# Kernel optimization log

Hardware: AMD Instinct MI355X
Metric: run time of the kernel (lower is better)

Reference implementation:

```python
import jax, jax.numpy as jnp
import numpy as np

NEG_SLOPE = 0.2
TAU_MRF = 1.0
N_NODES = 100000
PROJ_DIM = 128
GAT_DIM = 64
N_EDGES = 1000000


def setup_inputs() -> dict:
    key = jax.random.key(0)
    ks = jax.random.split(key, 8)
    z_beh = jax.random.normal(ks[0], (N_NODES, PROJ_DIM), dtype=jnp.float32)
    z_pref = jax.random.normal(ks[1], (N_NODES, PROJ_DIM), dtype=jnp.float32)
    edge_index = jax.random.randint(ks[2], (2, N_EDGES), 0, N_NODES, dtype=jnp.int64)
    # xavier_uniform for [GAT_DIM, PROJ_DIM] linear weights
    lim_w = float(np.sqrt(6.0 / (PROJ_DIM + GAT_DIM)))
    W_b = jax.random.uniform(ks[3], (GAT_DIM, PROJ_DIM), minval=-lim_w, maxval=lim_w, dtype=jnp.float32)
    W_p = jax.random.uniform(ks[4], (GAT_DIM, PROJ_DIM), minval=-lim_w, maxval=lim_w, dtype=jnp.float32)
    # xavier_uniform on view(1, 2D): fan_in=1? torch treats [1, 2D] -> fan_in=2D, fan_out=1
    lim_a = float(np.sqrt(6.0 / (1 + 2 * GAT_DIM)))
    a_b = jax.random.uniform(ks[5], (2 * GAT_DIM,), minval=-lim_a, maxval=lim_a, dtype=jnp.float32)
    a_p = jax.random.uniform(ks[6], (2 * GAT_DIM,), minval=-lim_a, maxval=lim_a, dtype=jnp.float32)
    gamma_b = jnp.zeros((), dtype=jnp.float32)
    gamma_p = jnp.zeros((), dtype=jnp.float32)
    return {"z_beh": z_beh, "z_pref": z_pref, "W_b": W_b, "W_p": W_p,
            "a_b": a_b, "a_p": a_p, "gamma_b": gamma_b, "gamma_p": gamma_p,
            "edge_index_undirected": edge_index}


def _sym_score(h, a, src, dst, neg_slope):
    # e_ij = leaky_relu((cat[h_src, h_dst]) . a). Split a to avoid materializing
    # the [E, 2D] concat: dot each node once, then gather scalars per edge.
    D = h.shape[-1]
    si = h @ a[:D]   # [N] contribution of left slot
    sj = h @ a[D:]   # [N] contribution of right slot
    e_ij = jax.nn.leaky_relu(si[src] + sj[dst], negative_slope=neg_slope)
    e_ji = jax.nn.leaky_relu(si[dst] + sj[src], negative_slope=neg_slope)
    return 0.5 * (e_ij + e_ji)


def reference(z_beh, z_pref, W_b, W_p, a_b, a_p, gamma_b, gamma_p, edge_index_undirected):
    src = edge_index_undirected[0]
    dst = edge_index_undirected[1]
    h_b = z_beh @ W_b.T   # [N, D]
    h_p = z_pref @ W_p.T  # [N, D]
    s_b = _sym_score(h_b, a_b, src, dst, NEG_SLOPE)  # [E]
    s_p = _sym_score(h_p, a_p, src, dst, NEG_SLOPE)  # [E]
    w = jax.nn.softmax(jnp.stack([gamma_b, gamma_p]))
    s = w[0] * s_b + w[1] * s_p
    alpha_ij = jax.nn.sigmoid(s / TAU_MRF)
    return alpha_ij
```

## Files before the change

kernel.cpp:

```cpp
#include <hip/hip_runtime.h>
#include <hip/hip_bf16.h>

#define NEG_SLOPE 0.2f

typedef float f32x4 __attribute__((ext_vector_type(4)));

__device__ __forceinline__ unsigned f2bf(float f) {
    unsigned u = __float_as_uint(f);
    return (u + 0x7FFFu + ((u >> 16) & 1u)) >> 16;
}
__device__ __forceinline__ float bf2f(unsigned h) {
    return __uint_as_float(h << 16);
}

__global__ void compute_v_kernel(const float* __restrict__ W_b,
                                 const float* __restrict__ W_p,
                                 const float* __restrict__ a_b,
                                 const float* __restrict__ a_p,
                                 float* __restrict__ v) {
    const int t  = threadIdx.x;
    const int p  = t & 127;
    const int ch = t >> 7;
    const float* W = ch ? W_p : W_b;
    const float* a = ch ? a_p : a_b;
    float acc1 = 0.f, acc2 = 0.f;
    #pragma unroll
    for (int d = 0; d < 64; ++d) {
        const float w = W[d * 128 + p];
        acc1 += w * a[d];
        acc2 += w * a[64 + d];
    }
    v[(2 * ch + 0) * 128 + p] = acc1;
    v[(2 * ch + 1) * 128 + p] = acc2;
}

__device__ __forceinline__ float fold_reduce(float sib, float sjb,
                                             float sip, float sjp,
                                             bool hiB, bool hiJ) {
    float g1 = hiB ? sib : sip;
    float r1 = __shfl_xor(g1, 16);
    float acc_i = (hiB ? sip : sib) + r1;
    float g2 = hiB ? sjb : sjp;
    float r2 = __shfl_xor(g2, 16);
    float acc_j = (hiB ? sjp : sjb) + r2;
    float g3 = hiJ ? acc_i : acc_j;
    float r3 = __shfl_xor(g3, 8);
    float acc = (hiJ ? acc_j : acc_i) + r3;
    acc += __shfl_xor(acc, 4);
    acc += __shfl_xor(acc, 2);
    acc += __shfl_xor(acc, 1);
    return acc;
}

__device__ __forceinline__ float dot4(const f32x4 z, const f32x4 v) {
    return z.x * v.x + z.y * v.y + z.z * v.z + z.w * v.w;
}

__device__ __forceinline__ void pack_store(float acc, int c, bool valid,
                                           uint2* __restrict__ tab8, int node) {
    const float a1 = __shfl_down(acc, 8);
    const float a2 = __shfl_down(acc, 16);
    const float a3 = __shfl_down(acc, 24);
    if (c == 0 && valid) {
        uint2 p;
        p.x = f2bf(acc) | (f2bf(a1) << 16);
        p.y = f2bf(a2) | (f2bf(a3) << 16);
        tab8[node] = p;
    }
}

__global__ void __launch_bounds__(256, 8) node_scores_kernel(
        const f32x4* __restrict__ zb4,
        const f32x4* __restrict__ zp4,
        const float* __restrict__ v,
        uint2*       __restrict__ tab8,
        int n_nodes) {
    const int tid  = threadIdx.x;
    const int lane = tid & 63;
    const int h    = lane >> 5;
    const int c    = lane & 31;
    const int wave   = (blockIdx.x * blockDim.x + tid) >> 6;
    const int nwaves = (gridDim.x * blockDim.x) >> 6;
    const int npairs = (n_nodes + 1) >> 1;

    const f32x4 v1b = *reinterpret_cast<const f32x4*>(v + 0 * 128 + 4 * c);
    const f32x4 v2b = *reinterpret_cast<const f32x4*>(v + 1 * 128 + 4 * c);
    const f32x4 v1p = *reinterpret_cast<const f32x4*>(v + 2 * 128 + 4 * c);
    const f32x4 v2p = *reinterpret_cast<const f32x4*>(v + 3 * 128 + 4 * c);

    const bool hiB = (c & 16) != 0;
    const bool hiJ = (c & 8)  != 0;

    for (int pr0 = wave; pr0 < npairs; pr0 += 4 * nwaves) {
        f32x4 zb[4], zp[4];
        #pragma unroll
        for (int j = 0; j < 4; ++j) {
            const int pr = pr0 + j * nwaves;
            if (pr < npairs) {
                const size_t base = (size_t)(2 * pr + h) * 32 + c;
                zb[j] = zb4[base];
                zp[j] = zp4[base];
            }
        }
        #pragma unroll
        for (int j = 0; j < 4; ++j) {
            const int pr = pr0 + j * nwaves;
            if (pr < npairs) {
                const int node = 2 * pr + h;
                const float acc = fold_reduce(
                    dot4(zb[j], v1b), dot4(zb[j], v2b),
                    dot4(zp[j], v1p), dot4(zp[j], v2p), hiB, hiJ);
                pack_store(acc, c, node < n_nodes, tab8, node);
            }
        }
    }
}

__device__ __forceinline__ float lrelu(float x) {
    return x >= 0.f ? x : NEG_SLOPE * x;
}

__device__ __forceinline__ float edge_score8(const uint2 ts, const uint2 td,
                                             float w0, float w1) {
    const float s_ib = bf2f(ts.x & 0xFFFFu), s_jb = bf2f(ts.x >> 16);
    const float s_ip = bf2f(ts.y & 0xFFFFu), s_jp = bf2f(ts.y >> 16);
    const float d_ib = bf2f(td.x & 0xFFFFu), d_jb = bf2f(td.x >> 16);
    const float d_ip = bf2f(td.y & 0xFFFFu), d_jp = bf2f(td.y >> 16);
    const float sb = 0.5f * (lrelu(s_ib + d_jb) + lrelu(d_ib + s_jb));
    const float sp = 0.5f * (lrelu(s_ip + d_jp) + lrelu(d_ip + s_jp));
    const float sc = w0 * sb + w1 * sp;
    return 1.f / (1.f + __expf(-sc));
}

__global__ void __launch_bounds__(256) edge_scores_kernel(
        const int*   __restrict__ src,
        const int*   __restrict__ dst,
        const uint2* __restrict__ tab8,
        const float* __restrict__ gamma_b,
        const float* __restrict__ gamma_p,
        float*       __restrict__ out,
        int n_edges) {
    const float gb = *gamma_b;
    const float gp = *gamma_p;
    const float w0 = 1.f / (1.f + __expf(gp - gb));
    const float w1 = 1.f - w0;

    const int n_half = n_edges >> 1;
    const int stride = gridDim.x * blockDim.x;
    const int gid    = blockIdx.x * blockDim.x + threadIdx.x;

    const int2* src2 = (const int2*)src;
    const int2* dst2 = (const int2*)dst;
    float2*     out2 = (float2*)out;

    for (int i = gid; i < n_half; i += stride) {
        const int2 s = src2[i];
        const int2 d = dst2[i];
        const uint2 ts0 = tab8[s.x];
        const uint2 td0 = tab8[d.x];
        const uint2 ts1 = tab8[s.y];
        const uint2 td1 = tab8[d.y];
        float2 r;
        r.x = edge_score8(ts0, td0, w0, w1);
        r.y = edge_score8(ts1, td1, w0, w1);
        out2[i] = r;
    }
    const int tail_base = n_half << 1;
    for (int e = tail_base + gid; e < n_edges; e += stride) {
        out[e] = edge_score8(tab8[src[e]], tab8[dst[e]], w0, w1);
    }
}

extern "C" void kernel_launch(void* const* d_in, const int* in_sizes, int n_in,
                              void* d_out, int out_size, void* d_ws, size_t ws_size,
                              hipStream_t stream) {
    const float* z_beh  = (const float*)d_in[0];
    const float* z_pref = (const float*)d_in[1];
    const float* W_b    = (const float*)d_in[2];
    const float* W_p    = (const float*)d_in[3];
    const float* a_b    = (const float*)d_in[4];
    const float* a_p    = (const float*)d_in[5];
    const float* g_b    = (const float*)d_in[6];
    const float* g_p    = (const float*)d_in[7];
    const int*   ei     = (const int*)d_in[8];

    const int n_nodes = in_sizes[0] / 128;
    const int n_edges = in_sizes[8] / 2;

    float* v    = (float*)d_ws;
    uint2* tab8 = (uint2*)((char*)d_ws + 2048);

    compute_v_kernel<<<1, 256, 0, stream>>>(W_b, W_p, a_b, a_p, v);

    node_scores_kernel<<<2048, 256, 0, stream>>>(
        (const f32x4*)z_beh, (const f32x4*)z_pref, v, tab8, n_nodes);

    const int n_half = n_edges >> 1;
    int eblocks = (n_half + 255) / 256;
    if (eblocks > 4096) eblocks = 4096;
    if (eblocks < 1) eblocks = 1;
    edge_scores_kernel<<<eblocks, 256, 0, stream>>>(
        ei, ei + n_edges, tab8, g_b, g_p, (float*)d_out, n_edges);
}
```

Before: 41.41 us.

## Fuse v-projection into node kernel and double-buffer z tiles via global_load_lds

Removes the separate single-block compute_v launch by having every node-score block recompute the projected attention vectors into shared memory. Node rows are staged into LDS with asynchronous global_load_lds DMA in a per-wave double buffer, so the load of the next 8-node tile overlaps compute on the current one. The reduction layout changes: each lane covers half of a row for one score vector and writes a single 16-bit entry. The cost is redundant W·a work in all 512 blocks, lower occupancy from 64KB of LDS per block, and four separate 2-byte stores per node instead of one packed 8-byte store.

```diff
diff --git a/kernel.cpp b/kernel.cpp
--- a/kernel.cpp
+++ b/kernel.cpp
@@ -1,5 +1,6 @@
 #include <hip/hip_runtime.h>
 #include <hip/hip_bf16.h>
+#include <stdint.h>
 
 #define NEG_SLOPE 0.2f
 
@@ -13,106 +14,100 @@
     return __uint_as_float(h << 16);
 }
 
-__global__ void compute_v_kernel(const float* __restrict__ W_b,
-                                 const float* __restrict__ W_p,
-                                 const float* __restrict__ a_b,
-                                 const float* __restrict__ a_p,
-                                 float* __restrict__ v) {
-    const int t  = threadIdx.x;
-    const int p  = t & 127;
-    const int ch = t >> 7;
-    const float* W = ch ? W_p : W_b;
-    const float* a = ch ? a_p : a_b;
-    float acc1 = 0.f, acc2 = 0.f;
-    #pragma unroll
-    for (int d = 0; d < 64; ++d) {
-        const float w = W[d * 128 + p];
-        acc1 += w * a[d];
-        acc2 += w * a[64 + d];
-    }
-    v[(2 * ch + 0) * 128 + p] = acc1;
-    v[(2 * ch + 1) * 128 + p] = acc2;
+__device__ __forceinline__ void dma16(const void* g, void* l) {
+    __builtin_amdgcn_global_load_lds(
+        (const __attribute__((address_space(1))) unsigned int*)g,
+        (__attribute__((address_space(3))) unsigned int*)l,
+        16, 0, 0);
 }
 
-__device__ __forceinline__ float fold_reduce(float sib, float sjb,
-                                             float sip, float sjp,
-                                             bool hiB, bool hiJ) {
-    float g1 = hiB ? sib : sip;
-    float r1 = __shfl_xor(g1, 16);
-    float acc_i = (hiB ? sip : sib) + r1;
-    float g2 = hiB ? sjb : sjp;
-    float r2 = __shfl_xor(g2, 16);
-    float acc_j = (hiB ? sjp : sjb) + r2;
-    float g3 = hiJ ? acc_i : acc_j;
-    float r3 = __shfl_xor(g3, 8);
-    float acc = (hiJ ? acc_j : acc_i) + r3;
-    acc += __shfl_xor(acc, 4);
-    acc += __shfl_xor(acc, 2);
-    acc += __shfl_xor(acc, 1);
-    return acc;
-}
-
-__device__ __forceinline__ float dot4(const f32x4 z, const f32x4 v) {
-    return z.x * v.x + z.y * v.y + z.z * v.z + z.w * v.w;
-}
-
-__device__ __forceinline__ void pack_store(float acc, int c, bool valid,
-                                           uint2* __restrict__ tab8, int node) {
-    const float a1 = __shfl_down(acc, 8);
-    const float a2 = __shfl_down(acc, 16);
-    const float a3 = __shfl_down(acc, 24);
-    if (c == 0 && valid) {
-        uint2 p;
-        p.x = f2bf(acc) | (f2bf(a1) << 16);
-        p.y = f2bf(a2) | (f2bf(a3) << 16);
-        tab8[node] = p;
-    }
-}
-
-__global__ void __launch_bounds__(256, 8) node_scores_kernel(
-        const f32x4* __restrict__ zb4,
-        const f32x4* __restrict__ zp4,
-        const float* __restrict__ v,
+__global__ void __launch_bounds__(256, 2) node_scores_kernel(
+        const float* __restrict__ W_b,
+        const float* __restrict__ W_p,
+        const float* __restrict__ a_b,
+        const float* __restrict__ a_p,
+        const char*  __restrict__ zb,
+        const char*  __restrict__ zp,
         uint2*       __restrict__ tab8,
         int n_nodes) {
-    const int tid  = threadIdx.x;
+    __shared__ float vsh[4][128];
+    __shared__ char  zbuf[4][2][8192];
+
+    const int tid = threadIdx.x;
+
+    {
+        const int p  = tid & 127;
+        const int ch = tid >> 7;
+        const float* W = ch ? W_p : W_b;
+        const float* a = ch ? a_p : a_b;
+        float acc1 = 0.f, acc2 = 0.f;
+        #pragma unroll
+        for (int d = 0; d < 64; ++d) {
+            const float w = W[d * 128 + p];
+            acc1 += w * a[d];
+            acc2 += w * a[64 + d];
+        }
+        vsh[2 * ch + 0][p] = acc1;
+        vsh[2 * ch + 1][p] = acc2;
+    }
+    __syncthreads();
+
+    const int wv   = tid >> 6;
     const int lane = tid & 63;
-    const int h    = lane >> 5;
-    const int c    = lane & 31;
+    const int ch   = lane >> 5;
+    const int n    = (lane >> 2) & 7;
+    const int comp = (lane >> 1) & 1;
+    const int half = lane & 1;
+    const int srow = n * 2 + half;
+    const int vec  = ch * 2 + comp;
+
+    const float* vrow = &vsh[vec][half * 64];
+    char* lb[2] = { &zbuf[wv][0][0], &zbuf[wv][1][0] };
+
+    const int dma_rch  = (lane >> 4);
+    const int dma_col  = (lane & 15) * 16;
+
+    const int nwaves = (gridDim.x * blockDim.x) >> 6;
+    const int ntiles = (n_nodes + 7) >> 3;
     const int wave   = (blockIdx.x * blockDim.x + tid) >> 6;
-    const int nwaves = (gridDim.x * blockDim.x) >> 6;
-    const int npairs = (n_nodes + 1) >> 1;
 
-    const f32x4 v1b = *reinterpret_cast<const f32x4*>(v + 0 * 128 + 4 * c);
-    const f32x4 v2b = *reinterpret_cast<const f32x4*>(v + 1 * 128 + 4 * c);
-    const f32x4 v1p = *reinterpret_cast<const f32x4*>(v + 2 * 128 + 4 * c);
-    const f32x4 v2p = *reinterpret_cast<const f32x4*>(v + 3 * 128 + 4 * c);
+    if (wave >= ntiles) return;
 
-    const bool hiB = (c & 16) != 0;
-    const bool hiJ = (c & 8)  != 0;
+    auto stage = [&](int b, int t) {
+        const size_t tb = (size_t)t * 4096;
+        #pragma unroll
+        for (int k = 0; k < 8; ++k) {
+            const char* gsrc = (k < 4) ? zb : zp;
+            const size_t g = tb + (size_t)((k & 3) * 4 + dma_rch) * 256 + dma_col;
+            dma16(gsrc + g, lb[b] + k * 1024);
+        }
+    };
 
-    for (int pr0 = wave; pr0 < npairs; pr0 += 4 * nwaves) {
-        f32x4 zb[4], zp[4];
+    stage(0, wave);
+    int buf = 0;
+    for (int t = wave; t < ntiles; t += nwaves) {
+        const int nx = t + nwaves;
+        stage(buf ^ 1, (nx < ntiles) ? nx : t);
+        asm volatile("s_waitcnt vmcnt(8)" ::: "memory");
+        __builtin_amdgcn_sched_barrier(0);
+
+        const char* zrow = lb[buf] + (ch * 16 + srow) * 256;
+        f32x4 acc4 = {0.f, 0.f, 0.f, 0.f};
         #pragma unroll
-        for (int j = 0; j < 4; ++j) {
-            const int pr = pr0 + j * nwaves;
-            if (pr < npairs) {
-                const size_t base = (size_t)(2 * pr + h) * 32 + c;
-                zb[j] = zb4[base];
-                zp[j] = zp4[base];
-            }
+        for (int m = 0; m < 16; ++m) {
+            const int slot = m ^ srow;
+            const f32x4 z4 = *(const f32x4*)(zrow + slot * 16);
+            const f32x4 v4 = *(const f32x4*)(vrow + slot * 4);
+            acc4 += z4 * v4;
         }
-        #pragma unroll
-        for (int j = 0; j < 4; ++j) {
-            const int pr = pr0 + j * nwaves;
-            if (pr < npairs) {
-                const int node = 2 * pr + h;
-                const float acc = fold_reduce(
-                    dot4(zb[j], v1b), dot4(zb[j], v2b),
-                    dot4(zp[j], v1p), dot4(zp[j], v2p), hiB, hiJ);
-                pack_store(acc, c, node < n_nodes, tab8, node);
-            }
+        float acc = acc4.x + acc4.y + acc4.z + acc4.w;
+        acc += __shfl_xor(acc, 1);
+        const int node = t * 8 + n;
+        if (half == 0 && node < n_nodes) {
+            unsigned short* t16 = (unsigned short*)&tab8[node];
+            t16[vec] = (unsigned short)f2bf(acc);
         }
+        buf ^= 1;
     }
 }
 
@@ -187,13 +182,11 @@
     const int n_nodes = in_sizes[0] / 128;
     const int n_edges = in_sizes[8] / 2;
 
-    float* v    = (float*)d_ws;
-    uint2* tab8 = (uint2*)((char*)d_ws + 2048);
+    uint2* tab8 = (uint2*)d_ws;
 
-    compute_v_kernel<<<1, 256, 0, stream>>>(W_b, W_p, a_b, a_p, v);
-
-    node_scores_kernel<<<2048, 256, 0, stream>>>(
-        (const f32x4*)z_beh, (const f32x4*)z_pref, v, tab8, n_nodes);
+    node_scores_kernel<<<512, 256, 0, stream>>>(
+        W_b, W_p, a_b, a_p,
+        (const char*)z_beh, (const char*)z_pref, tab8, n_nodes);
 
     const int n_half = n_edges >> 1;
     int eblocks = (n_half + 255) / 256;
```

Result: faster. 36.49 us (-11.9%).
